# Kernel optimization log

Hardware: AMD Instinct MI355X
Metric: run time of the kernel (lower is better)

The kernel has to match this reference:

```python
import jax, jax.numpy as jnp
import numpy as np

N_NODES = 50000
N_EDGES = 800000
DIM_IN = 64
DIM_H = 32
HEADS = 4
NUM_CLASSES = 10
NEG_SLOPE = 0.2  # DGL GATv2Conv default negative_slope


def _gatv2_layer(x, W_src, b_src, W_dst, b_dst, attn, src, dst):
    """DGL GATv2Conv (share_weights=False, eval mode so feat_drop is identity).
    x: [N, F_in]; attn: [H, D]; returns [N, H, D]."""
    N = x.shape[0]
    H, D = attn.shape
    fs = (x @ W_src + b_src).reshape(N, H, D)  # source projection
    fd = (x @ W_dst + b_dst).reshape(N, H, D)  # destination projection
    # per-edge additive attention: leaky_relu(fs[u] + fd[v]) . attn  -> [E, H]
    e = jax.nn.leaky_relu(fs[src] + fd[dst], NEG_SLOPE)  # [E, H, D]
    s = jnp.einsum('ehd,hd->eh', e, attn)  # [E, H]
    # edge softmax over incoming edges of each destination node
    smax = jax.lax.stop_gradient(
        jax.ops.segment_max(s, dst, num_segments=N))  # [N, H]
    es = jnp.exp(s - smax[dst])
    denom = jax.ops.segment_sum(es, dst, num_segments=N)  # [N, H]
    alpha = es / denom[dst]
    # weighted scatter-aggregate of source features
    out = jax.ops.segment_sum(alpha[:, :, None] * fs[src], dst, num_segments=N)
    return out  # [N, H, D]


def setup_inputs() -> dict:
    key = jax.random.key(0)
    ks = jax.random.split(key, 16)
    sc = 0.05
    inp = {
        'g_feats': jax.random.normal(ks[0], (N_NODES, DIM_IN), jnp.float32),
        'edge_src': jax.random.randint(ks[1], (N_EDGES,), 0, N_NODES, jnp.int32),
        'edge_dst': jax.random.randint(ks[2], (N_EDGES,), 0, N_NODES, jnp.int32),
        # input embedding Linear(dim_in, dim_h)
        'W_in': jax.random.normal(ks[3], (DIM_IN, DIM_H), jnp.float32) * sc,
        'b_in': jnp.zeros((DIM_H,), jnp.float32),
        # GATv2 layer 1: Linear(dim_h, heads*dim_h) for src/dst + attn [H, D]
        'W1_src': jax.random.normal(ks[4], (DIM_H, HEADS * DIM_H), jnp.float32) * sc,
        'b1_src': jnp.zeros((HEADS * DIM_H,), jnp.float32),
        'W1_dst': jax.random.normal(ks[5], (DIM_H, HEADS * DIM_H), jnp.float32) * sc,
        'b1_dst': jnp.zeros((HEADS * DIM_H,), jnp.float32),
        'attn1': jax.random.normal(ks[6], (HEADS, DIM_H), jnp.float32) * sc,
        # GATv2 layer 2
        'W2_src': jax.random.normal(ks[7], (DIM_H, HEADS * DIM_H), jnp.float32) * sc,
        'b2_src': jnp.zeros((HEADS * DIM_H,), jnp.float32),
        'W2_dst': jax.random.normal(ks[8], (DIM_H, HEADS * DIM_H), jnp.float32) * sc,
        'b2_dst': jnp.zeros((HEADS * DIM_H,), jnp.float32),
        'attn2': jax.random.normal(ks[9], (HEADS, DIM_H), jnp.float32) * sc,
        # MLP head: Linear(dim_h, dim_h) -> relu -> (dropout: eval) -> Linear(dim_h, num_classes)
        'Wh1': jax.random.normal(ks[10], (DIM_H, DIM_H), jnp.float32) * sc,
        'bh1': jnp.zeros((DIM_H,), jnp.float32),
        'Wh2': jax.random.normal(ks[11], (DIM_H, NUM_CLASSES), jnp.float32) * sc,
        'bh2': jnp.zeros((NUM_CLASSES,), jnp.float32),
    }
    return inp


def reference(g_feats, W_in, b_in,
              W1_src, b1_src, W1_dst, b1_dst, attn1,
              W2_src, b2_src, W2_dst, b2_dst, attn2,
              Wh1, bh1, Wh2, bh2,
              edge_src, edge_dst):
    x = g_feats @ W_in + b_in  # input embedding, [N, dim_h]
    h = _gatv2_layer(x, W1_src, b1_src, W1_dst, b1_dst, attn1, edge_src, edge_dst)
    h = jax.nn.relu(h.mean(axis=1))  # mean over heads -> [N, dim_h]
    h = _gatv2_layer(h, W2_src, b2_src, W2_dst, b2_dst, attn2, edge_src, edge_dst)
    h = h.mean(axis=1)  # [N, dim_h]
    # dgl.readout_nodes(op='mean') over the single graph -> [1, dim_h]
    g = h.mean(axis=0, keepdims=True)
    g = jax.nn.relu(g @ Wh1 + bh1)  # head (dropout inactive in eval)
    logits = g @ Wh2 + bh2
    return jax.nn.softmax(logits, axis=-1)  # [1, num_classes]
```

## Files before the change

kernel.cpp:

```cpp
#include <hip/hip_runtime.h>
#include <hip/hip_bf16.h>

#define N_NODES 50000
#define N_EDGES 800000
#define DIM_IN 64
#define DIM_H 32
#define HEADS 4
#define NCLS 10
#define NEG 0.2f
#define NBUCK 196
#define NPW 25
#define FSCALE 16.0f

typedef float floatx2 __attribute__((ext_vector_type(2)));


__global__ void k_bhist(const int* __restrict__ dst, int* __restrict__ bh) {
    __shared__ int lh[NBUCK];
    for (int i = threadIdx.x; i < NBUCK; i += 256) lh[i] = 0;
    __syncthreads();
    int base = blockIdx.x * 1024 + threadIdx.x;
#pragma unroll
    for (int r = 0; r < 4; r++) {
        int e = base + r * 256;
        if (e < N_EDGES) atomicAdd(&lh[dst[e] >> 8], 1);
    }
    __syncthreads();
    for (int i = threadIdx.x; i < NBUCK; i += 256) {
        int c = lh[i];
        if (c) atomicAdd(&bh[i], c);
    }
}

__global__ void k_bscan(const int* __restrict__ bh, int* __restrict__ bbase,
                        int* __restrict__ gcur) {
    __shared__ int s[256];
    int t = threadIdx.x;
    int v = (t < NBUCK) ? bh[t] : 0;
    s[t] = v;
    __syncthreads();
    for (int off = 1; off < 256; off <<= 1) {
        int u = (t >= off) ? s[t - off] : 0;
        __syncthreads();
        s[t] += u;
        __syncthreads();
    }
    int excl = s[t] - v;
    if (t < NBUCK) {
        bbase[t] = excl;
        gcur[t] = excl;
    }
    if (t == 0) bbase[NBUCK] = N_EDGES;
}

__global__ void k_bin(const int* __restrict__ src, const int* __restrict__ dst,
                      int* __restrict__ gcur, unsigned* __restrict__ stage) {
    __shared__ int lh[NBUCK], chunk[NBUCK];
    int t = threadIdx.x;
    for (int i = t; i < NBUCK; i += 256) lh[i] = 0;
    __syncthreads();
    int e0 = blockIdx.x * 4096;
    unsigned pk[16];
    int bk[16];
#pragma unroll
    for (int r = 0; r < 16; r++) {
        int e = e0 + r * 256 + t;
        bool ok = e < N_EDGES;
        int s = ok ? src[e] : 0;
        int d = ok ? dst[e] : 0;
        bk[r] = ok ? (d >> 8) : -1;
        pk[r] = (unsigned)s | ((unsigned)(d & 255) << 16);
        if (ok) atomicAdd(&lh[bk[r]], 1);
    }
    __syncthreads();
    for (int i = t; i < NBUCK; i += 256) {
        int c = lh[i];
        chunk[i] = c ? atomicAdd(&gcur[i], c) : 0;
        lh[i] = 0;
    }
    __syncthreads();
#pragma unroll
    for (int r = 0; r < 16; r++) {
        if (bk[r] >= 0) {
            int lp = atomicAdd(&lh[bk[r]], 1);
            stage[chunk[bk[r]] + lp] = pk[r];
        }
    }
}

__global__ void k_csr(const unsigned* __restrict__ stage, const int* __restrict__ bbase,
                      int* __restrict__ row, unsigned short* __restrict__ adj) {
    __shared__ int lcnt[256], lcur[256], sc[256];
    int b = blockIdx.x, t = threadIdx.x;
    int s0 = bbase[b], s1 = bbase[b + 1];
    lcnt[t] = 0;
    __syncthreads();
    for (int i = s0 + t; i < s1; i += 256) atomicAdd(&lcnt[stage[i] >> 16], 1);
    __syncthreads();
    int v = lcnt[t];
    sc[t] = v;
    __syncthreads();
    for (int off = 1; off < 256; off <<= 1) {
        int u = (t >= off) ? sc[t - off] : 0;
        __syncthreads();
        sc[t] += u;
        __syncthreads();
    }
    int excl = sc[t] - v;
    int n = b * 256 + t;
    if (n < N_NODES) row[n] = s0 + excl;
    if (b == NBUCK - 1 && t == 0) row[N_NODES] = N_EDGES;
    lcur[t] = s0 + excl;
    __syncthreads();
    for (int i = s0 + t; i < s1; i += 256) {
        unsigned p = stage[i];
        int pos = atomicAdd(&lcur[p >> 16], 1);
        adj[pos] = (unsigned short)(p & 0xFFFFu);
    }
}

__global__ __launch_bounds__(256, 2) void k_fused1(
    const float* __restrict__ gf, const float* __restrict__ W_in,
    const float* __restrict__ b_in, const float* __restrict__ W1s,
    const float* __restrict__ b1s, const float* __restrict__ W1d,
    const float* __restrict__ b1d, unsigned char* __restrict__ fsh,
    float* __restrict__ fd) {
    __shared__ float4 xb[4][2][8];
    int lane = threadIdx.x & 63;
    int wvl = threadIdx.x >> 6;
    int wave = (blockIdx.x * 256 + threadIdx.x) >> 6;
    int c = lane & 31, h = lane >> 5;
    int n0 = wave * NPW;
    if (n0 >= N_NODES) return;
    float wi[32];
#pragma unroll
    for (int k = 0; k < 32; k++) wi[k] = W_in[(h * 32 + k) * DIM_H + c];
    float bc = b_in[c];
    const float4* Wb = (lane < 32) ? (const float4*)W1s : (const float4*)W1d;
    const float4* bb = (lane < 32) ? (const float4*)b1s : (const float4*)b1d;
    float4 w[32];
#pragma unroll
    for (int k = 0; k < 32; k++) w[k] = Wb[k * 32 + c];
    float4 bias = bb[c];
#pragma unroll 2
    for (int i = 0; i < NPW; i++) {
        int nu = __builtin_amdgcn_readfirstlane(n0 + i);
        const float4* gr = (const float4*)(gf + (size_t)nu * DIM_IN + h * 32);
        float a1 = 0.f;
#pragma unroll
        for (int k4 = 0; k4 < 8; k4++) {
            float4 xv = gr[k4];
            a1 += xv.x * wi[k4 * 4 + 0];
            a1 += xv.y * wi[k4 * 4 + 1];
            a1 += xv.z * wi[k4 * 4 + 2];
            a1 += xv.w * wi[k4 * 4 + 3];
        }
        a1 += __shfl_xor(a1, 32, 64);
        if (lane < 32) ((float*)&xb[wvl][i & 1][0])[c] = a1 + bc;
        float4 acc = bias;
#pragma unroll
        for (int k4 = 0; k4 < 8; k4++) {
            float4 xv = xb[wvl][i & 1][k4];
#pragma unroll
            for (int j = 0; j < 4; j++) {
                float xk = (j == 0) ? xv.x : (j == 1) ? xv.y : (j == 2) ? xv.z : xv.w;
                float4 wk = w[k4 * 4 + j];
                acc.x += xk * wk.x;
                acc.y += xk * wk.y;
                acc.z += xk * wk.z;
                acc.w += xk * wk.w;
            }
        }
        if (lane < 32) {
            int pk = __builtin_amdgcn_cvt_pk_fp8_f32(acc.x * FSCALE, acc.y * FSCALE,
                                                     0, false);
            pk = __builtin_amdgcn_cvt_pk_fp8_f32(acc.z * FSCALE, acc.w * FSCALE,
                                                 pk, true);
            *(int*)&fsh[(size_t)nu * 128 + c * 4] = pk;
        } else {
            float4 o;
            o.x = acc.x * FSCALE;
            o.y = acc.y * FSCALE;
            o.z = acc.z * FSCALE;
            o.w = acc.w * FSCALE;
            *(float4*)&fd[(size_t)nu * 128 + c * 4] = o;
        }
    }
}

__global__ __launch_bounds__(256, 2) void k_proj(
    const float* __restrict__ x, const float* __restrict__ Wsrc,
    const float* __restrict__ bsrc, const float* __restrict__ Wdst,
    const float* __restrict__ bdst, unsigned char* __restrict__ fsh,
    float* __restrict__ fd) {
    int lane = threadIdx.x & 63;
    int wave = (blockIdx.x * 256 + threadIdx.x) >> 6;
    int cl = lane & 31;
    int n0 = wave * NPW;
    if (n0 >= N_NODES) return;
    const float4* Wb = (lane < 32) ? (const float4*)Wsrc : (const float4*)Wdst;
    const float4* bb = (lane < 32) ? (const float4*)bsrc : (const float4*)bdst;
    float4 w[32];
#pragma unroll
    for (int k = 0; k < 32; k++) w[k] = Wb[k * 32 + cl];
    float4 bias = bb[cl];
#pragma unroll 2
    for (int i = 0; i < NPW; i++) {
        int nu = __builtin_amdgcn_readfirstlane(n0 + i);
        const float4* xr = (const float4*)(x + (size_t)nu * DIM_H);
        float4 acc = bias;
#pragma unroll
        for (int k4 = 0; k4 < 8; k4++) {
            float4 xv = xr[k4];
#pragma unroll
            for (int j = 0; j < 4; j++) {
                float xk = (j == 0) ? xv.x : (j == 1) ? xv.y : (j == 2) ? xv.z : xv.w;
                float4 wk = w[k4 * 4 + j];
                acc.x += xk * wk.x;
                acc.y += xk * wk.y;
                acc.z += xk * wk.z;
                acc.w += xk * wk.w;
            }
        }
        if (lane < 32) {
            int pk = __builtin_amdgcn_cvt_pk_fp8_f32(acc.x * FSCALE, acc.y * FSCALE,
                                                     0, false);
            pk = __builtin_amdgcn_cvt_pk_fp8_f32(acc.z * FSCALE, acc.w * FSCALE,
                                                 pk, true);
            *(int*)&fsh[(size_t)nu * 128 + cl * 4] = pk;
        } else {
            float4 o;
            o.x = acc.x * FSCALE;
            o.y = acc.y * FSCALE;
            o.z = acc.z * FSCALE;
            o.w = acc.w * FSCALE;
            *(float4*)&fd[(size_t)nu * 128 + cl * 4] = o;
        }
    }
}

__device__ __forceinline__ void pair_acc(unsigned u, const float4& fdv,
                                         const float4& a4, float4& acc, float& den,
                                         bool valid) {
    floatx2 f01 = __builtin_amdgcn_cvt_pk_f32_fp8((int)u, false);
    floatx2 f23 = __builtin_amdgcn_cvt_pk_f32_fp8((int)u, true);
    float t0 = f01.x + fdv.x; t0 = fmaxf(t0, NEG * t0);
    float t1 = f01.y + fdv.y; t1 = fmaxf(t1, NEG * t1);
    float t2 = f23.x + fdv.z; t2 = fmaxf(t2, NEG * t2);
    float t3 = f23.y + fdv.w; t3 = fmaxf(t3, NEG * t3);
    float p = t0 * a4.x + t1 * a4.y + t2 * a4.z + t3 * a4.w;
    p += __shfl_xor(p, 1, 64);
    p += __shfl_xor(p, 2, 64);
    p += __shfl_xor(p, 4, 64);
    float w = __expf(p);
    if (!valid) w = 0.f;
    den += w;
    acc.x += w * f01.x;
    acc.y += w * f01.y;
    acc.z += w * f23.x;
    acc.w += w * f23.y;
}

__global__ void k_gather(const unsigned char* __restrict__ fsh,
                         const float* __restrict__ fd, const float* __restrict__ attn,
                         const int* __restrict__ row,
                         const unsigned short* __restrict__ adj,
                         float* __restrict__ xout, float* __restrict__ gpart,
                         int mode) {
    __shared__ float bsum[32];
    int tid = threadIdx.x;
    if (mode) {
        if (tid < 32) bsum[tid] = 0.f;
        __syncthreads();
    }
    int wave = tid >> 6;
    int lane = tid & 63;
    int n = blockIdx.x * 4 + wave;
    int sub = lane & 31, e2 = lane >> 5;
    unsigned suboff = (unsigned)sub << 2;
    float4 a4 = ((const float4*)attn)[sub];
    a4.x *= (1.f / FSCALE);
    a4.y *= (1.f / FSCALE);
    a4.z *= (1.f / FSCALE);
    a4.w *= (1.f / FSCALE);
    float4 fdv = ((const float4*)(fd + (size_t)n * 128))[sub];
    float4 acc = {0.f, 0.f, 0.f, 0.f};
    float den = 0.f;
    int beg = row[n], end = row[n + 1];
    for (int base = beg; base < end; base += 64) {
        int m = end - base;
        if (m > 64) m = 64;
        int myadj = (lane < m) ? (int)adj[base + lane] : 0;
        int j = 0;
        for (; j + 8 <= m; j += 8) {
            unsigned o0 = ((unsigned)__shfl(myadj, j + 0 + e2, 64) << 7) + suboff;
            unsigned o1 = ((unsigned)__shfl(myadj, j + 2 + e2, 64) << 7) + suboff;
            unsigned o2 = ((unsigned)__shfl(myadj, j + 4 + e2, 64) << 7) + suboff;
            unsigned o3 = ((unsigned)__shfl(myadj, j + 6 + e2, 64) << 7) + suboff;
            unsigned u0 = *(const unsigned*)(fsh + o0);
            unsigned u1 = *(const unsigned*)(fsh + o1);
            unsigned u2 = *(const unsigned*)(fsh + o2);
            unsigned u3 = *(const unsigned*)(fsh + o3);
            pair_acc(u0, fdv, a4, acc, den, true);
            pair_acc(u1, fdv, a4, acc, den, true);
            pair_acc(u2, fdv, a4, acc, den, true);
            pair_acc(u3, fdv, a4, acc, den, true);
        }
        for (; j < m; j += 2) {
            int idx = j + e2;
            bool valid = idx < m;
            unsigned o = ((unsigned)__shfl(myadj, valid ? idx : j, 64) << 7) + suboff;
            unsigned u = *(const unsigned*)(fsh + o);
            pair_acc(u, fdv, a4, acc, den, valid);
        }
    }
    den += __shfl_xor(den, 32, 64);
    acc.x += __shfl_xor(acc.x, 32, 64);
    acc.y += __shfl_xor(acc.y, 32, 64);
    acc.z += __shfl_xor(acc.z, 32, 64);
    acc.w += __shfl_xor(acc.w, 32, 64);
    float inv = den > 0.f ? (0.25f / FSCALE) / den : 0.f;
    float4 o;
    o.x = acc.x * inv;
    o.y = acc.y * inv;
    o.z = acc.z * inv;
    o.w = acc.w * inv;
    o.x += __shfl_xor(o.x, 8, 64);
    o.y += __shfl_xor(o.y, 8, 64);
    o.z += __shfl_xor(o.z, 8, 64);
    o.w += __shfl_xor(o.w, 8, 64);
    o.x += __shfl_xor(o.x, 16, 64);
    o.y += __shfl_xor(o.y, 16, 64);
    o.z += __shfl_xor(o.z, 16, 64);
    o.w += __shfl_xor(o.w, 16, 64);
    if (mode == 0) {
        if (lane < 8) {
            o.x = fmaxf(o.x, 0.f);
            o.y = fmaxf(o.y, 0.f);
            o.z = fmaxf(o.z, 0.f);
            o.w = fmaxf(o.w, 0.f);
            ((float4*)(xout + (size_t)n * 32))[lane] = o;
        }
    } else {
        if (lane < 8) {
            atomicAdd(&bsum[lane * 4 + 0], o.x);
            atomicAdd(&bsum[lane * 4 + 1], o.y);
            atomicAdd(&bsum[lane * 4 + 2], o.z);
            atomicAdd(&bsum[lane * 4 + 3], o.w);
        }
        __syncthreads();
        if (tid < 32) atomicAdd(&gpart[(blockIdx.x & 63) * 32 + tid], bsum[tid]);
    }
}

__global__ void k_final(const float* __restrict__ gpart, const float* __restrict__ Wh1,
                        const float* __restrict__ bh1, const float* __restrict__ Wh2,
                        const float* __restrict__ bh2, float* __restrict__ out) {
    __shared__ float gv[32], gh[32], lg[16];
    int t = threadIdx.x;
    if (t < 32) {
        float s = 0.f;
        for (int b = 0; b < 64; b++) s += gpart[b * 32 + t];
        gv[t] = s * (1.f / (float)N_NODES);
    }
    __syncthreads();
    if (t < 32) {
        float s = bh1[t];
        for (int d = 0; d < 32; d++) s += gv[d] * Wh1[d * 32 + t];
        gh[t] = s > 0.f ? s : 0.f;
    }
    __syncthreads();
    if (t < NCLS) {
        float s = bh2[t];
        for (int j = 0; j < 32; j++) s += gh[j] * Wh2[j * NCLS + t];
        lg[t] = s;
    }
    __syncthreads();
    if (t == 0) {
        float m = lg[0];
        for (int c = 1; c < NCLS; c++) m = fmaxf(m, lg[c]);
        float ex[NCLS], sum = 0.f;
        for (int c = 0; c < NCLS; c++) {
            ex[c] = __expf(lg[c] - m);
            sum += ex[c];
        }
        float inv = 1.f / sum;
        for (int c = 0; c < NCLS; c++) out[c] = ex[c] * inv;
    }
}

extern "C" void kernel_launch(void* const* d_in, const int* in_sizes, int n_in,
                              void* d_out, int out_size, void* d_ws, size_t ws_size,
                              hipStream_t stream) {
    const float* g_feats = (const float*)d_in[0];
    const int* edge_src = (const int*)d_in[1];
    const int* edge_dst = (const int*)d_in[2];
    const float* W_in = (const float*)d_in[3];
    const float* b_in = (const float*)d_in[4];
    const float* W1_src = (const float*)d_in[5];
    const float* b1_src = (const float*)d_in[6];
    const float* W1_dst = (const float*)d_in[7];
    const float* b1_dst = (const float*)d_in[8];
    const float* attn1 = (const float*)d_in[9];
    const float* W2_src = (const float*)d_in[10];
    const float* b2_src = (const float*)d_in[11];
    const float* W2_dst = (const float*)d_in[12];
    const float* b2_dst = (const float*)d_in[13];
    const float* attn2 = (const float*)d_in[14];
    const float* Wh1 = (const float*)d_in[15];
    const float* bh1 = (const float*)d_in[16];
    const float* Wh2 = (const float*)d_in[17];
    const float* bh2 = (const float*)d_in[18];

    float* x = (float*)d_ws;
    unsigned char* fsh = (unsigned char*)(x + (size_t)N_NODES * 32);
    float* fd = (float*)(fsh + (size_t)N_NODES * 128);
    float* gpart = fd + (size_t)N_NODES * 128;
    int* bh = (int*)(gpart + 64 * 32);
    int* bbase = bh + NBUCK;
    int* gcur = bbase + NBUCK + 1;
    int* row = gcur + NBUCK;
    unsigned* stage = (unsigned*)(row + N_NODES + 1);
    unsigned short* adj = (unsigned short*)(stage + N_EDGES);

    const int WB = (N_NODES / NPW + 3) / 4;

    hipMemsetAsync(gpart, 0, (64 * 32 + NBUCK) * sizeof(int), stream);

    k_bhist<<<(N_EDGES + 1023) / 1024, 256, 0, stream>>>(edge_dst, bh);
    k_bscan<<<1, 256, 0, stream>>>(bh, bbase, gcur);
    k_bin<<<(N_EDGES + 4095) / 4096, 256, 0, stream>>>(edge_src, edge_dst, gcur, stage);
    k_csr<<<NBUCK, 256, 0, stream>>>(stage, bbase, row, adj);

    k_fused1<<<WB, 256, 0, stream>>>(g_feats, W_in, b_in, W1_src, b1_src, W1_dst,
                                     b1_dst, fsh, fd);
    k_gather<<<N_NODES / 4, 256, 0, stream>>>(fsh, fd, attn1, row, adj, x, gpart, 0);

    k_proj<<<WB, 256, 0, stream>>>(x, W2_src, b2_src, W2_dst, b2_dst, fsh, fd);
    k_gather<<<N_NODES / 4, 256, 0, stream>>>(fsh, fd, attn2, row, adj, x, gpart, 1);

    k_final<<<1, 256, 0, stream>>>(gpart, Wh1, bh1, Wh2, bh2, (float*)d_out);
}
```

Baseline: 186.4 us.

## Store dst projections in bf16, use exp2 and packed math in gather

The destination projection buffer is written as bf16 instead of fp32, which halves its storage and the write and read traffic for it. The gather kernel folds log2(e) into the attention scale so it can call a native exp2. It also rewrites the per-edge math with two-wide float vectors so the compiler can emit packed FP32 operations. An unrolled path now handles 16 edges per iteration to keep more gather loads in flight, at the cost of more registers and extra bf16 rounding error in the attention logits.

```diff
diff --git a/kernel.cpp b/kernel.cpp
--- a/kernel.cpp
+++ b/kernel.cpp
@@ -11,8 +11,17 @@
 #define NBUCK 196
 #define NPW 25
 #define FSCALE 16.0f
+#define LOG2E 1.44269504088896f
 
 typedef float floatx2 __attribute__((ext_vector_type(2)));
+
+__device__ __forceinline__ float fast_exp2(float x) {
+#if __has_builtin(__builtin_amdgcn_exp2f)
+    return __builtin_amdgcn_exp2f(x);
+#else
+    return __expf(x * 0.69314718055994531f);
+#endif
+}
 
 
 __global__ void k_bhist(const int* __restrict__ dst, int* __restrict__ bh) {
@@ -119,12 +128,22 @@
     }
 }
 
+
+__device__ __forceinline__ unsigned short f2bf(float v) {
+    unsigned u = __builtin_bit_cast(unsigned, v);
+    u += 0x7FFFu + ((u >> 16) & 1u);
+    return (unsigned short)(u >> 16);
+}
+__device__ __forceinline__ float bf2f(unsigned short h) {
+    return __builtin_bit_cast(float, (unsigned)h << 16);
+}
+
 __global__ __launch_bounds__(256, 2) void k_fused1(
     const float* __restrict__ gf, const float* __restrict__ W_in,
     const float* __restrict__ b_in, const float* __restrict__ W1s,
     const float* __restrict__ b1s, const float* __restrict__ W1d,
     const float* __restrict__ b1d, unsigned char* __restrict__ fsh,
-    float* __restrict__ fd) {
+    unsigned short* __restrict__ fdh) {
     __shared__ float4 xb[4][2][8];
     int lane = threadIdx.x & 63;
     int wvl = threadIdx.x >> 6;
@@ -178,12 +197,12 @@
                                                  pk, true);
             *(int*)&fsh[(size_t)nu * 128 + c * 4] = pk;
         } else {
-            float4 o;
-            o.x = acc.x * FSCALE;
-            o.y = acc.y * FSCALE;
-            o.z = acc.z * FSCALE;
-            o.w = acc.w * FSCALE;
-            *(float4*)&fd[(size_t)nu * 128 + c * 4] = o;
+            ushort4 o;
+            o.x = f2bf(acc.x * FSCALE);
+            o.y = f2bf(acc.y * FSCALE);
+            o.z = f2bf(acc.z * FSCALE);
+            o.w = f2bf(acc.w * FSCALE);
+            *(ushort4*)&fdh[(size_t)nu * 128 + c * 4] = o;
         }
     }
 }
@@ -192,7 +211,7 @@
     const float* __restrict__ x, const float* __restrict__ Wsrc,
     const float* __restrict__ bsrc, const float* __restrict__ Wdst,
     const float* __restrict__ bdst, unsigned char* __restrict__ fsh,
-    float* __restrict__ fd) {
+    unsigned short* __restrict__ fdh) {
     int lane = threadIdx.x & 63;
     int wave = (blockIdx.x * 256 + threadIdx.x) >> 6;
     int cl = lane & 31;
@@ -229,41 +248,46 @@
                                                  pk, true);
             *(int*)&fsh[(size_t)nu * 128 + cl * 4] = pk;
         } else {
-            float4 o;
-            o.x = acc.x * FSCALE;
-            o.y = acc.y * FSCALE;
-            o.z = acc.z * FSCALE;
-            o.w = acc.w * FSCALE;
-            *(float4*)&fd[(size_t)nu * 128 + cl * 4] = o;
-        }
-    }
-}
-
-__device__ __forceinline__ void pair_acc(unsigned u, const float4& fdv,
-                                         const float4& a4, float4& acc, float& den,
-                                         bool valid) {
+            ushort4 o;
+            o.x = f2bf(acc.x * FSCALE);
+            o.y = f2bf(acc.y * FSCALE);
+            o.z = f2bf(acc.z * FSCALE);
+            o.w = f2bf(acc.w * FSCALE);
+            *(ushort4*)&fdh[(size_t)nu * 128 + cl * 4] = o;
+        }
+    }
+}
+
+__device__ __forceinline__ void pair_acc(unsigned u, floatx2 fd01, floatx2 fd23,
+                                         floatx2 a01, floatx2 a23, floatx2& acc01,
+                                         floatx2& acc23, float& den, bool valid) {
     floatx2 f01 = __builtin_amdgcn_cvt_pk_f32_fp8((int)u, false);
     floatx2 f23 = __builtin_amdgcn_cvt_pk_f32_fp8((int)u, true);
-    float t0 = f01.x + fdv.x; t0 = fmaxf(t0, NEG * t0);
-    float t1 = f01.y + fdv.y; t1 = fmaxf(t1, NEG * t1);
-    float t2 = f23.x + fdv.z; t2 = fmaxf(t2, NEG * t2);
-    float t3 = f23.y + fdv.w; t3 = fmaxf(t3, NEG * t3);
-    float p = t0 * a4.x + t1 * a4.y + t2 * a4.z + t3 * a4.w;
+    floatx2 t01 = f01 + fd01;
+    floatx2 t23 = f23 + fd23;
+    floatx2 n01 = t01 * NEG;
+    floatx2 n23 = t23 * NEG;
+    floatx2 l01, l23;
+    l01.x = fmaxf(t01.x, n01.x);
+    l01.y = fmaxf(t01.y, n01.y);
+    l23.x = fmaxf(t23.x, n23.x);
+    l23.y = fmaxf(t23.y, n23.y);
+    floatx2 d = l01 * a01 + l23 * a23;
+    float p = d.x + d.y;
     p += __shfl_xor(p, 1, 64);
     p += __shfl_xor(p, 2, 64);
     p += __shfl_xor(p, 4, 64);
-    float w = __expf(p);
+    float w = fast_exp2(p);
     if (!valid) w = 0.f;
     den += w;
-    acc.x += w * f01.x;
-    acc.y += w * f01.y;
-    acc.z += w * f23.x;
-    acc.w += w * f23.y;
+    floatx2 wv = {w, w};
+    acc01 += wv * f01;
+    acc23 += wv * f23;
 }
 
 __global__ void k_gather(const unsigned char* __restrict__ fsh,
-                         const float* __restrict__ fd, const float* __restrict__ attn,
-                         const int* __restrict__ row,
+                         const unsigned short* __restrict__ fdh,
+                         const float* __restrict__ attn, const int* __restrict__ row,
                          const unsigned short* __restrict__ adj,
                          float* __restrict__ xout, float* __restrict__ gpart,
                          int mode) {
@@ -279,12 +303,13 @@
     int sub = lane & 31, e2 = lane >> 5;
     unsigned suboff = (unsigned)sub << 2;
     float4 a4 = ((const float4*)attn)[sub];
-    a4.x *= (1.f / FSCALE);
-    a4.y *= (1.f / FSCALE);
-    a4.z *= (1.f / FSCALE);
-    a4.w *= (1.f / FSCALE);
-    float4 fdv = ((const float4*)(fd + (size_t)n * 128))[sub];
-    float4 acc = {0.f, 0.f, 0.f, 0.f};
+    const float asc = LOG2E / FSCALE;
+    floatx2 a01 = {a4.x * asc, a4.y * asc};
+    floatx2 a23 = {a4.z * asc, a4.w * asc};
+    ushort4 fdu = *(const ushort4*)(fdh + (size_t)n * 128 + sub * 4);
+    floatx2 fd01 = {bf2f(fdu.x), bf2f(fdu.y)};
+    floatx2 fd23 = {bf2f(fdu.z), bf2f(fdu.w)};
+    floatx2 acc01 = {0.f, 0.f}, acc23 = {0.f, 0.f};
     float den = 0.f;
     int beg = row[n], end = row[n + 1];
     for (int base = beg; base < end; base += 64) {
@@ -292,6 +317,32 @@
         if (m > 64) m = 64;
         int myadj = (lane < m) ? (int)adj[base + lane] : 0;
         int j = 0;
+        for (; j + 16 <= m; j += 16) {
+            unsigned o0 = ((unsigned)__shfl(myadj, j + 0 + e2, 64) << 7) + suboff;
+            unsigned o1 = ((unsigned)__shfl(myadj, j + 2 + e2, 64) << 7) + suboff;
+            unsigned o2 = ((unsigned)__shfl(myadj, j + 4 + e2, 64) << 7) + suboff;
+            unsigned o3 = ((unsigned)__shfl(myadj, j + 6 + e2, 64) << 7) + suboff;
+            unsigned o4 = ((unsigned)__shfl(myadj, j + 8 + e2, 64) << 7) + suboff;
+            unsigned o5 = ((unsigned)__shfl(myadj, j + 10 + e2, 64) << 7) + suboff;
+            unsigned o6 = ((unsigned)__shfl(myadj, j + 12 + e2, 64) << 7) + suboff;
+            unsigned o7 = ((unsigned)__shfl(myadj, j + 14 + e2, 64) << 7) + suboff;
+            unsigned u0 = *(const unsigned*)(fsh + o0);
+            unsigned u1 = *(const unsigned*)(fsh + o1);
+            unsigned u2 = *(const unsigned*)(fsh + o2);
+            unsigned u3 = *(const unsigned*)(fsh + o3);
+            unsigned u4 = *(const unsigned*)(fsh + o4);
+            unsigned u5 = *(const unsigned*)(fsh + o5);
+            unsigned u6 = *(const unsigned*)(fsh + o6);
+            unsigned u7 = *(const unsigned*)(fsh + o7);
+            pair_acc(u0, fd01, fd23, a01, a23, acc01, acc23, den, true);
+            pair_acc(u1, fd01, fd23, a01, a23, acc01, acc23, den, true);
+            pair_acc(u2, fd01, fd23, a01, a23, acc01, acc23, den, true);
+            pair_acc(u3, fd01, fd23, a01, a23, acc01, acc23, den, true);
+            pair_acc(u4, fd01, fd23, a01, a23, acc01, acc23, den, true);
+            pair_acc(u5, fd01, fd23, a01, a23, acc01, acc23, den, true);
+            pair_acc(u6, fd01, fd23, a01, a23, acc01, acc23, den, true);
+            pair_acc(u7, fd01, fd23, a01, a23, acc01, acc23, den, true);
+        }
         for (; j + 8 <= m; j += 8) {
             unsigned o0 = ((unsigned)__shfl(myadj, j + 0 + e2, 64) << 7) + suboff;
             unsigned o1 = ((unsigned)__shfl(myadj, j + 2 + e2, 64) << 7) + suboff;
@@ -301,30 +352,31 @@
             unsigned u1 = *(const unsigned*)(fsh + o1);
             unsigned u2 = *(const unsigned*)(fsh + o2);
             unsigned u3 = *(const unsigned*)(fsh + o3);
-            pair_acc(u0, fdv, a4, acc, den, true);
-            pair_acc(u1, fdv, a4, acc, den, true);
-            pair_acc(u2, fdv, a4, acc, den, true);
-            pair_acc(u3, fdv, a4, acc, den, true);
+            pair_acc(u0, fd01, fd23, a01, a23, acc01, acc23, den, true);
+            pair_acc(u1, fd01, fd23, a01, a23, acc01, acc23, den, true);
+            pair_acc(u2, fd01, fd23, a01, a23, acc01, acc23, den, true);
+            pair_acc(u3, fd01, fd23, a01, a23, acc01, acc23, den, true);
         }
         for (; j < m; j += 2) {
             int idx = j + e2;
             bool valid = idx < m;
             unsigned o = ((unsigned)__shfl(myadj, valid ? idx : j, 64) << 7) + suboff;
             unsigned u = *(const unsigned*)(fsh + o);
-            pair_acc(u, fdv, a4, acc, den, valid);
+            pair_acc(u, fd01, fd23, a01, a23, acc01, acc23, den, valid);
         }
     }
     den += __shfl_xor(den, 32, 64);
-    acc.x += __shfl_xor(acc.x, 32, 64);
-    acc.y += __shfl_xor(acc.y, 32, 64);
-    acc.z += __shfl_xor(acc.z, 32, 64);
-    acc.w += __shfl_xor(acc.w, 32, 64);
+    float ax = acc01.x, ay = acc01.y, az = acc23.x, aw = acc23.y;
+    ax += __shfl_xor(ax, 32, 64);
+    ay += __shfl_xor(ay, 32, 64);
+    az += __shfl_xor(az, 32, 64);
+    aw += __shfl_xor(aw, 32, 64);
     float inv = den > 0.f ? (0.25f / FSCALE) / den : 0.f;
     float4 o;
-    o.x = acc.x * inv;
-    o.y = acc.y * inv;
-    o.z = acc.z * inv;
-    o.w = acc.w * inv;
+    o.x = ax * inv;
+    o.y = ay * inv;
+    o.z = az * inv;
+    o.w = aw * inv;
     o.x += __shfl_xor(o.x, 8, 64);
     o.y += __shfl_xor(o.y, 8, 64);
     o.z += __shfl_xor(o.z, 8, 64);
@@ -414,8 +466,8 @@
 
     float* x = (float*)d_ws;
     unsigned char* fsh = (unsigned char*)(x + (size_t)N_NODES * 32);
-    float* fd = (float*)(fsh + (size_t)N_NODES * 128);
-    float* gpart = fd + (size_t)N_NODES * 128;
+    unsigned short* fdh = (unsigned short*)(fsh + (size_t)N_NODES * 128);
+    float* gpart = (float*)(fdh + (size_t)N_NODES * 128);
     int* bh = (int*)(gpart + 64 * 32);
     int* bbase = bh + NBUCK;
     int* gcur = bbase + NBUCK + 1;
@@ -433,11 +485,11 @@
     k_csr<<<NBUCK, 256, 0, stream>>>(stage, bbase, row, adj);
 
     k_fused1<<<WB, 256, 0, stream>>>(g_feats, W_in, b_in, W1_src, b1_src, W1_dst,
-                                     b1_dst, fsh, fd);
-    k_gather<<<N_NODES / 4, 256, 0, stream>>>(fsh, fd, attn1, row, adj, x, gpart, 0);
-
-    k_proj<<<WB, 256, 0, stream>>>(x, W2_src, b2_src, W2_dst, b2_dst, fsh, fd);
-    k_gather<<<N_NODES / 4, 256, 0, stream>>>(fsh, fd, attn2, row, adj, x, gpart, 1);
+                                     b1_dst, fsh, fdh);
+    k_gather<<<N_NODES / 4, 256, 0, stream>>>(fsh, fdh, attn1, row, adj, x, gpart, 0);
+
+    k_proj<<<WB, 256, 0, stream>>>(x, W2_src, b2_src, W2_dst, b2_dst, fsh, fdh);
+    k_gather<<<N_NODES / 4, 256, 0, stream>>>(fsh, fdh, attn2, row, adj, x, gpart, 1);
 
     k_final<<<1, 256, 0, stream>>>(gpart, Wh1, bh1, Wh2, bh2, (float*)d_out);
 }
```

Measured after the change: 184.3 us, median of 3. About the same (-1.1%).
